# Performance work log

Measured on AMD Instinct MI355X. Metric: run time of the kernel, lower is better.

## Reference

```python
import jax, jax.numpy as jnp
import numpy as np

T, B, N, R, E, D = 20, 4, 50000, 4, 1600000, 5
DT = 1.0

@jax.custom_vjp
def spike(v_scaled, dampening):
    # Heaviside spike with surrogate (triangular pseudo-derivative) gradient
    return (v_scaled > 0.0).astype(v_scaled.dtype)

def _spike_fwd(v_scaled, dampening):
    return spike(v_scaled, dampening), (v_scaled, dampening)

def _spike_bwd(res, g):
    v_scaled, dampening = res
    dz_dv = dampening * jnp.maximum(1.0 - jnp.abs(v_scaled), 0.0)
    return (g * dz_dv, jnp.zeros_like(dampening))

spike.defvjp(_spike_fwd, _spike_bwd)


def setup_inputs() -> dict:
    key = jax.random.key(0)
    ks = jax.random.split(key, 16)
    return {
        'x': 0.1 * jax.random.normal(ks[0], (T, B, N, R), jnp.float32),
        'weights': 0.02 * jax.random.normal(ks[1], (E,), jnp.float32),
        'syn_decay': 0.6 + 0.35 * jax.random.uniform(ks[2], (N, R), jnp.float32),
        'psc_initial': 0.1 + 0.9 * jax.random.uniform(ks[3], (N, R), jnp.float32),
        'asc_amps': -0.1 * jax.random.uniform(ks[4], (N, 2), jnp.float32),
        'exp_k1': 0.7 + 0.25 * jax.random.uniform(ks[5], (N,), jnp.float32),
        'exp_k2': 0.8 + 0.15 * jax.random.uniform(ks[6], (N,), jnp.float32),
        'decay': 0.7 + 0.25 * jax.random.uniform(ks[7], (N,), jnp.float32),
        'current_factor': 0.2 + 0.3 * jax.random.uniform(ks[8], (N,), jnp.float32),
        'v_th': jnp.ones((N,), jnp.float32),          # normalized V_th = 1
        'e_l': jnp.zeros((N,), jnp.float32),          # normalized E_L = 0
        'v_reset': jnp.zeros((N,), jnp.float32),      # normalized V_reset = 0
        't_ref': 1.0 + 2.0 * jax.random.uniform(ks[9], (N,), jnp.float32),
        'param_g': 0.5 + jax.random.uniform(ks[10], (N,), jnp.float32),
        'dampening': jnp.asarray(0.3, jnp.float32),
        'rows': jax.random.randint(ks[11], (E,), 0, N * R, jnp.int32),   # post*R + receptor slot
        'cols': jax.random.randint(ks[12], (E,), 0, N * D, jnp.int32),   # pre + N*(delay-1)
    }


def reference(x, weights, syn_decay, psc_initial, asc_amps, exp_k1, exp_k2,
              decay, current_factor, v_th, e_l, v_reset, t_ref, param_g,
              dampening, rows, cols):
    normalizer = v_th - e_l
    v_gap = v_reset - v_th
    gathered_g = param_g * e_l

    def step(carry, x_t):
        z_buf, v, r, asc1, asc2, psc_rise, psc = carry
        prev_z = z_buf[:, :N]                                  # most recent spikes [B,N]
        # sparse recurrent gather-multiply-scatter: [B,E] -> segment_sum -> [B,N*R]
        vals = weights[None, :] * z_buf[:, cols]
        rec = jax.ops.segment_sum(vals.T, rows, num_segments=N * R).T
        inp = rec.reshape(B, N, R) + x_t                       # receptor-resolved drive
        # double-exponential synapse per receptor channel
        new_psc_rise = syn_decay * psc_rise + psc_initial * inp
        new_psc = psc * syn_decay + DT * syn_decay * psc_rise
        input_current = new_psc.sum(-1)                        # [B,N]
        # after-spike currents (GLIF3)
        new_asc1 = exp_k1 * asc1 + prev_z * asc_amps[:, 0]
        new_asc2 = exp_k2 * asc2 + prev_z * asc_amps[:, 1]
        c1 = input_current + asc1 + asc2 + gathered_g
        new_v = decay * v + current_factor * c1 + prev_z * v_gap  # soft reset
        v_sc = (new_v - v_th) / normalizer
        new_z = spike(v_sc, dampening)
        new_z = jnp.where(r > 0.0, 0.0, new_z)                 # refractory clamp
        new_r = jax.lax.stop_gradient(jnp.clip(r + new_z * t_ref - DT, 0.0, t_ref))
        new_z_buf = jnp.concatenate([new_z, z_buf[:, :-N]], axis=1)
        return (new_z_buf, new_v, new_r, new_asc1, new_asc2, new_psc_rise, new_psc), new_z

    zero = jnp.zeros((B, N), jnp.float32)
    init = (jnp.zeros((B, N * D), jnp.float32),
            zero + e_l[None, :], zero, zero, zero,
            jnp.zeros((B, N, R), jnp.float32), jnp.zeros((B, N, R), jnp.float32))
    _, spikes = jax.lax.scan(step, init, x)
    return spikes  # [T,B,N]
```

## Files before the change

kernel.cpp:

```cpp
#include <hip/hip_runtime.h>

namespace {
constexpr int TS = 20;
constexpr int B  = 4;
constexpr int N  = 50000;
constexpr int R  = 4;
constexpr int E  = 1600000;
constexpr int D  = 5;
constexpr int NR = N * R;
constexpr float DT = 1.0f;

typedef float f32x4 __attribute__((ext_vector_type(4)));

constexpr size_t OFF_ZPACK = 0;
constexpr size_t OFF_CNT   = 250112;
constexpr size_t OFF_REC   = 262144;
constexpr size_t OFF_RBUF  = OFF_REC  + (size_t)B * N * R * 4;
constexpr size_t OFF_ASC1  = OFF_RBUF + (size_t)B * N * 4;
constexpr size_t OFF_ASC2  = OFF_ASC1 + (size_t)B * N * 4;
constexpr size_t OFF_PR    = OFF_ASC2 + (size_t)B * N * 4;
constexpr size_t OFF_PC    = OFF_PR   + (size_t)B * N * R * 4;
constexpr size_t OFF_V     = OFF_PC   + (size_t)B * N * R * 4;
constexpr size_t ZERO_BYTES = OFF_V;
}

__global__ __launch_bounds__(256) void vinit_kernel(float* __restrict__ v,
                                                    const float* __restrict__ e_l) {
  int i = blockIdx.x * 256 + threadIdx.x;
  if (i < B * N) v[i] = e_l[i % N];
}

__global__ __launch_bounds__(256) void gather_kernel(const int4* __restrict__ cols4,
                                                     const int* __restrict__ rows,
                                                     const float* __restrict__ weights,
                                                     const unsigned char* __restrict__ zpack,
                                                     float* __restrict__ rec,
                                                     const int* __restrict__ cnt_win,
                                                     int head) {
  int tot = cnt_win[0] + cnt_win[1] + cnt_win[2] + cnt_win[3] + cnt_win[4];
  if (tot == 0) return;

  int q = blockIdx.x * 256 + threadIdx.x;
  if (q >= E / 4) return;
  const int4 c4 = cols4[q];

#pragma unroll
  for (int j = 0; j < 4; ++j) {
    const int c = (j == 0) ? c4.x : (j == 1) ? c4.y : (j == 2) ? c4.z : c4.w;
    int d = c / N;
    int n = c - d * N;
    int slot = head + d; if (slot >= D) slot -= D;
    const unsigned char m = zpack[slot * N + n];
    if (m) {
      const int e = q * 4 + j;
      const float w = weights[e];
      const int row = rows[e];
      if (m & 1) atomicAdd(rec + 0 * NR + row, w);
      if (m & 2) atomicAdd(rec + 1 * NR + row, w);
      if (m & 4) atomicAdd(rec + 2 * NR + row, w);
      if (m & 8) atomicAdd(rec + 3 * NR + row, w);
    }
  }
}

__global__ __launch_bounds__(256) void neuron_kernel(
    const f32x4* __restrict__ x_t,
    const float4* __restrict__ syn_decay,
    const float4* __restrict__ psc_init,
    const float2* __restrict__ asc_amps,
    const float* __restrict__ exp_k1, const float* __restrict__ exp_k2,
    const float* __restrict__ decay,  const float* __restrict__ cur_fac,
    const float* __restrict__ v_th,   const float* __restrict__ e_l,
    const float* __restrict__ v_reset,const float* __restrict__ t_ref,
    const float* __restrict__ param_g,
    float4* __restrict__ rec,
    float*  __restrict__ v,    float* __restrict__ rbuf,
    float*  __restrict__ asc1, float* __restrict__ asc2,
    float4* __restrict__ psc_rise, float4* __restrict__ psc,
    unsigned char* __restrict__ zpack,
    int* __restrict__ cnt_t,
    int head, int newslot,
    float* __restrict__ out_t) {
  int n = blockIdx.x * 256 + threadIdx.x;
  if (n >= N) return;

  const float4 sd  = syn_decay[n];
  const float4 pi  = psc_init[n];
  const float2 amp = asc_amps[n];
  const float k1n = exp_k1[n], k2n = exp_k2[n];
  const float dec = decay[n],  cfn = cur_fac[n];
  const float vth = v_th[n],   eln = e_l[n];
  const float vrs = v_reset[n], trf = t_ref[n], pg = param_g[n];
  const float norm = vth - eln;
  const float vgap = vrs - vth;
  const float gg   = pg * eln;

  const unsigned char prevmask = zpack[head * N + n];
  unsigned char newmask = 0;

#pragma unroll
  for (int b = 0; b < B; ++b) {
    const int bn = b * N + n;
    float4 pr = psc_rise[bn];
    float4 pc = psc[bn];
    float4 rc = rec[bn];
    rec[bn] = make_float4(0.f, 0.f, 0.f, 0.f);
    f32x4 xx = __builtin_nontemporal_load(x_t + bn);

    float ix = rc.x + xx.x, iy = rc.y + xx.y, iz = rc.z + xx.z, iw = rc.w + xx.w;
    float4 npc = { sd.x * pc.x + sd.x * pr.x,
                   sd.y * pc.y + sd.y * pr.y,
                   sd.z * pc.z + sd.z * pr.z,
                   sd.w * pc.w + sd.w * pr.w };
    float4 npr = { sd.x * pr.x + pi.x * ix,
                   sd.y * pr.y + pi.y * iy,
                   sd.z * pr.z + pi.z * iz,
                   sd.w * pr.w + pi.w * iw };
    psc[bn] = npc;
    psc_rise[bn] = npr;

    const float I = npc.x + npc.y + npc.z + npc.w;
    const float pz = (prevmask >> b) & 1 ? 1.0f : 0.0f;

    float a1 = asc1[bn];
    float a2 = asc2[bn];
    const float c1 = I + a1 + a2 + gg;
    asc1[bn] = k1n * a1 + pz * amp.x;
    asc2[bn] = k2n * a2 + pz * amp.y;

    const float vo = v[bn];
    const float vn = dec * vo + cfn * c1 + pz * vgap;
    v[bn] = vn;

    const float vsc = (vn - vth) / norm;
    float z = (vsc > 0.f) ? 1.0f : 0.0f;
    const float rr = rbuf[bn];
    if (rr > 0.f) z = 0.0f;
    float rn = rr + z * trf - DT;
    rn = fminf(fmaxf(rn, 0.f), trf);
    rbuf[bn] = rn;

    __builtin_nontemporal_store(z, &out_t[bn]);
    newmask |= (unsigned char)((z != 0.f) ? (1 << b) : 0);
  }
  zpack[newslot * N + n] = newmask;
  if (newmask) atomicAdd(cnt_t, 1);
}

extern "C" void kernel_launch(void* const* d_in, const int* in_sizes, int n_in,
                              void* d_out, int out_size, void* d_ws, size_t ws_size,
                              hipStream_t stream) {
  const float* x        = (const float*)d_in[0];
  const float* weights  = (const float*)d_in[1];
  const float* syn_dec  = (const float*)d_in[2];
  const float* psc_init = (const float*)d_in[3];
  const float* asc_amps = (const float*)d_in[4];
  const float* exp_k1   = (const float*)d_in[5];
  const float* exp_k2   = (const float*)d_in[6];
  const float* decay    = (const float*)d_in[7];
  const float* cur_fac  = (const float*)d_in[8];
  const float* v_th     = (const float*)d_in[9];
  const float* e_l      = (const float*)d_in[10];
  const float* v_reset  = (const float*)d_in[11];
  const float* t_ref    = (const float*)d_in[12];
  const float* param_g  = (const float*)d_in[13];
  const int* rows       = (const int*)d_in[15];
  const int* cols       = (const int*)d_in[16];

  char* ws = (char*)d_ws;
  unsigned char* zpack = (unsigned char*)(ws + OFF_ZPACK);
  int*   cnt   = (int*)(ws + OFF_CNT);
  float* rec   = (float*)(ws + OFF_REC);
  float* rbuf  = (float*)(ws + OFF_RBUF);
  float* asc1  = (float*)(ws + OFF_ASC1);
  float* asc2  = (float*)(ws + OFF_ASC2);
  float* prise = (float*)(ws + OFF_PR);
  float* psc   = (float*)(ws + OFF_PC);
  float* v     = (float*)(ws + OFF_V);
  float* out   = (float*)d_out;

  (void)hipMemsetAsync(ws, 0, ZERO_BYTES, stream);
  vinit_kernel<<<(B * N + 255) / 256, 256, 0, stream>>>(v, e_l);

  const int gather_blocks = (E / 4 + 255) / 256;
  const int neuron_blocks = (N + 255) / 256;

  for (int t = 0; t < TS; ++t) {
    const int head    = (D - (t % D)) % D;
    const int newslot = (head + D - 1) % D;

    gather_kernel<<<gather_blocks, 256, 0, stream>>>((const int4*)cols, rows, weights,
                                                     zpack, rec, cnt + t, head);

    neuron_kernel<<<neuron_blocks, 256, 0, stream>>>(
        (const f32x4*)(x + (size_t)t * B * N * R),
        (const float4*)syn_dec, (const float4*)psc_init, (const float2*)asc_amps,
        exp_k1, exp_k2, decay, cur_fac, v_th, e_l, v_reset, t_ref, param_g,
        (float4*)rec, v, rbuf, asc1, asc2,
        (float4*)prise, (float4*)psc,
        zpack, cnt + t + D, head, newslot,
        out + (size_t)t * B * N);
  }
}
```

Before: 652.7 us.

## Interleave batch into neuron state layout and use one thread per (neuron,batch)

State arrays (v, rbuf, asc, psc, rec) are reorganized from batch-major to neuron-major with the batch index innermost, and the neuron kernel now uses one thread per (neuron, batch) pair instead of looping over the batch. The spike mask for the delay buffer is assembled with a wavefront ballot. In the gather kernel, the four batch atomics for one row now land in adjacent cache lines. The aim is more parallelism in the neuron step and better atomic locality. The cost is redundant per-neuron parameter loads across the four batch threads and strided x/out accesses.

Measured after the change: 951.0 us. 1.46x slower.

```diff
diff --git a/kernel.cpp b/kernel.cpp
--- a/kernel.cpp
+++ b/kernel.cpp
@@ -27,7 +27,7 @@
 __global__ __launch_bounds__(256) void vinit_kernel(float* __restrict__ v,
                                                     const float* __restrict__ e_l) {
   int i = blockIdx.x * 256 + threadIdx.x;
-  if (i < B * N) v[i] = e_l[i % N];
+  if (i < B * N) v[i] = e_l[i >> 2];
 }
 
 __global__ __launch_bounds__(256) void gather_kernel(const int4* __restrict__ cols4,
@@ -55,10 +55,11 @@
       const int e = q * 4 + j;
       const float w = weights[e];
       const int row = rows[e];
-      if (m & 1) atomicAdd(rec + 0 * NR + row, w);
-      if (m & 2) atomicAdd(rec + 1 * NR + row, w);
-      if (m & 4) atomicAdd(rec + 2 * NR + row, w);
-      if (m & 8) atomicAdd(rec + 3 * NR + row, w);
+      float* base = rec + ((row & ~3) << 2) + (row & 3);
+      if (m & 1) atomicAdd(base + 0, w);
+      if (m & 2) atomicAdd(base + 4, w);
+      if (m & 4) atomicAdd(base + 8, w);
+      if (m & 8) atomicAdd(base + 12, w);
     }
   }
 }
@@ -81,8 +82,10 @@
     int* __restrict__ cnt_t,
     int head, int newslot,
     float* __restrict__ out_t) {
-  int n = blockIdx.x * 256 + threadIdx.x;
-  if (n >= N) return;
+  const int idx = blockIdx.x * 256 + threadIdx.x;
+  if (idx >= B * N) return;
+  const int n = idx >> 2;
+  const int b = idx & 3;
 
   const float4 sd  = syn_decay[n];
   const float4 pi  = psc_init[n];
@@ -95,56 +98,55 @@
   const float vgap = vrs - vth;
   const float gg   = pg * eln;
 
-  const unsigned char prevmask = zpack[head * N + n];
-  unsigned char newmask = 0;
-
-#pragma unroll
-  for (int b = 0; b < B; ++b) {
-    const int bn = b * N + n;
-    float4 pr = psc_rise[bn];
-    float4 pc = psc[bn];
-    float4 rc = rec[bn];
-    rec[bn] = make_float4(0.f, 0.f, 0.f, 0.f);
-    f32x4 xx = __builtin_nontemporal_load(x_t + bn);
-
-    float ix = rc.x + xx.x, iy = rc.y + xx.y, iz = rc.z + xx.z, iw = rc.w + xx.w;
-    float4 npc = { sd.x * pc.x + sd.x * pr.x,
-                   sd.y * pc.y + sd.y * pr.y,
-                   sd.z * pc.z + sd.z * pr.z,
-                   sd.w * pc.w + sd.w * pr.w };
-    float4 npr = { sd.x * pr.x + pi.x * ix,
-                   sd.y * pr.y + pi.y * iy,
-                   sd.z * pr.z + pi.z * iz,
-                   sd.w * pr.w + pi.w * iw };
-    psc[bn] = npc;
-    psc_rise[bn] = npr;
-
-    const float I = npc.x + npc.y + npc.z + npc.w;
-    const float pz = (prevmask >> b) & 1 ? 1.0f : 0.0f;
-
-    float a1 = asc1[bn];
-    float a2 = asc2[bn];
-    const float c1 = I + a1 + a2 + gg;
-    asc1[bn] = k1n * a1 + pz * amp.x;
-    asc2[bn] = k2n * a2 + pz * amp.y;
-
-    const float vo = v[bn];
-    const float vn = dec * vo + cfn * c1 + pz * vgap;
-    v[bn] = vn;
-
-    const float vsc = (vn - vth) / norm;
-    float z = (vsc > 0.f) ? 1.0f : 0.0f;
-    const float rr = rbuf[bn];
-    if (rr > 0.f) z = 0.0f;
-    float rn = rr + z * trf - DT;
-    rn = fminf(fmaxf(rn, 0.f), trf);
-    rbuf[bn] = rn;
-
-    __builtin_nontemporal_store(z, &out_t[bn]);
-    newmask |= (unsigned char)((z != 0.f) ? (1 << b) : 0);
+  const float pz = (zpack[head * N + n] >> b) & 1 ? 1.0f : 0.0f;
+
+  float4 pr = psc_rise[idx];
+  float4 pc = psc[idx];
+  float4 rc = rec[idx];
+  rec[idx] = make_float4(0.f, 0.f, 0.f, 0.f);
+  f32x4 xx = __builtin_nontemporal_load(x_t + (b * N + n));
+
+  const float ix = rc.x + xx.x, iy = rc.y + xx.y, iz = rc.z + xx.z, iw = rc.w + xx.w;
+  float4 npc = { sd.x * pc.x + sd.x * pr.x,
+                 sd.y * pc.y + sd.y * pr.y,
+                 sd.z * pc.z + sd.z * pr.z,
+                 sd.w * pc.w + sd.w * pr.w };
+  float4 npr = { sd.x * pr.x + pi.x * ix,
+                 sd.y * pr.y + pi.y * iy,
+                 sd.z * pr.z + pi.z * iz,
+                 sd.w * pr.w + pi.w * iw };
+  psc[idx] = npc;
+  psc_rise[idx] = npr;
+
+  const float I = npc.x + npc.y + npc.z + npc.w;
+
+  const float a1 = asc1[idx];
+  const float a2 = asc2[idx];
+  const float c1 = I + a1 + a2 + gg;
+  asc1[idx] = k1n * a1 + pz * amp.x;
+  asc2[idx] = k2n * a2 + pz * amp.y;
+
+  const float vo = v[idx];
+  const float vn = dec * vo + cfn * c1 + pz * vgap;
+  v[idx] = vn;
+
+  const float vsc = (vn - vth) / norm;
+  float z = (vsc > 0.f) ? 1.0f : 0.0f;
+  const float rr = rbuf[idx];
+  if (rr > 0.f) z = 0.0f;
+  float rn = rr + z * trf - DT;
+  rn = fminf(fmaxf(rn, 0.f), trf);
+  rbuf[idx] = rn;
+
+  __builtin_nontemporal_store(z, &out_t[b * N + n]);
+
+  const unsigned long long bal = __ballot(z != 0.f);
+  if (b == 0) {
+    const unsigned lane = threadIdx.x & 63;
+    const unsigned char m = (unsigned char)((bal >> (lane & ~3u)) & 0xFull);
+    zpack[newslot * N + n] = m;
+    if (m) atomicAdd(cnt_t, 1);
   }
-  zpack[newslot * N + n] = newmask;
-  if (newmask) atomicAdd(cnt_t, 1);
 }
 
 extern "C" void kernel_launch(void* const* d_in, const int* in_sizes, int n_in,
@@ -183,7 +185,7 @@
   vinit_kernel<<<(B * N + 255) / 256, 256, 0, stream>>>(v, e_l);
 
   const int gather_blocks = (E / 4 + 255) / 256;
-  const int neuron_blocks = (N + 255) / 256;
+  const int neuron_blocks = (B * N + 255) / 256;
 
   for (int t = 0; t < TS; ++t) {
     const int head    = (D - (t % D)) % D;
```
